# Kernel tuning notes

Measured on AMD Instinct MI355X. Metric: run time of the kernel, lower is better.

Reference implementation:

```python
import jax, jax.numpy as jnp
import numpy as np

B, S, IN, OUT, GS = 4, 2048, 4096, 4096, 256
NG = IN // GS  # number of groups per output channel


def setup_inputs() -> dict:
    key = jax.random.key(0)
    k1, k2, k3, k4 = jax.random.split(key, 4)
    x = jax.random.normal(k1, (B, S, IN), dtype=jnp.float32)
    # int4 codes stored in int8: values in [-8, 7]
    weight_int8 = jax.random.randint(k2, (OUT, IN), -8, 8, dtype=jnp.int32).astype(jnp.int8)
    scales = jax.random.uniform(k3, (OUT, NG), dtype=jnp.float32, minval=0.001, maxval=0.02)
    # zero points stored in scales_precision (float), integer-valued in int4 range
    zeros = jax.random.randint(k4, (OUT, NG), -8, 8, dtype=jnp.int32).astype(jnp.float32)
    return {"x": x, "weight_int8": weight_int8, "scales": scales, "zeros": zeros,
            "group_size": GS}


def per_token_dynamic_quant(x):
    """Asymmetric per-token int8 quantize -> dequantize (torchao decomposed ops)."""
    qmin, qmax = -128.0, 127.0
    mn = jnp.minimum(jnp.min(x, axis=-1, keepdims=True), 0.0)
    mx = jnp.maximum(jnp.max(x, axis=-1, keepdims=True), 0.0)
    eps = jnp.finfo(jnp.float32).eps
    scale = jnp.maximum((mx - mn) / (qmax - qmin), eps)
    # choose zero point minimizing error at whichever end is larger
    zp = jnp.where((qmin + mn / scale) + (qmax + mx / scale) > 0,
                   qmin - mn / scale, qmax - mx / scale)
    zp = jnp.clip(jnp.round(zp), qmin, qmax)
    q = jnp.clip(jnp.round(x / scale) + zp, qmin, qmax)
    return (q - zp) * scale


def dequant_per_channel_group(w_int8, scales, zeros, group_size):
    O, I = w_int8.shape
    g = I // group_size
    w = w_int8.reshape(O, g, group_size).astype(jnp.float32)
    w_dq = (w - zeros[:, :, None]) * scales[:, :, None]
    return w_dq.reshape(O, I)


def reference(x, weight_int8, scales, zeros, group_size):
    xq = per_token_dynamic_quant(x.astype(jnp.float32))
    w_dq = dequant_per_channel_group(weight_int8, scales, zeros, group_size)
    # F.linear: x @ w_dq.T  -> [B, S, OUT]
    return jnp.einsum('bsi,oi->bso', xq, w_dq)
```

## Files before the change

kernel.cpp:

```cpp
#include <hip/hip_runtime.h>
#include <hip/hip_bf16.h>
#include <stdint.h>

#define T_   8192
#define IN_  4096
#define OUT_ 4096
#define GS_  256
#define NG_  16

#define BM 128
#define BN 128
#define BK 128
#define KT (IN_ / BK)

typedef int   v4i __attribute__((ext_vector_type(4)));
typedef float f4  __attribute__((ext_vector_type(4)));

__device__ __forceinline__ void gload16(const void* g, void* l) {
  __builtin_amdgcn_global_load_lds(
      (const __attribute__((address_space(1))) void*)g,
      (__attribute__((address_space(3))) void*)l, 16, 0, 0);
}

__global__ __launch_bounds__(256) void quant_kernel(
    const float* __restrict__ x, int8_t* __restrict__ q,
    float* __restrict__ tscale, float* __restrict__ tzp) {
  const int t = blockIdx.x;
  const int tid = threadIdx.x;
  const float* xr = x + (size_t)t * IN_ + tid * 16;
  float vals[16];
  {
    f4 v0 = *(const f4*)(xr);
    f4 v1 = *(const f4*)(xr + 4);
    f4 v2 = *(const f4*)(xr + 8);
    f4 v3 = *(const f4*)(xr + 12);
#pragma unroll
    for (int i = 0; i < 4; ++i) {
      vals[i] = v0[i]; vals[4 + i] = v1[i]; vals[8 + i] = v2[i]; vals[12 + i] = v3[i];
    }
  }
  float mn = 0.f, mx = 0.f;
#pragma unroll
  for (int i = 0; i < 16; ++i) { mn = fminf(mn, vals[i]); mx = fmaxf(mx, vals[i]); }
#pragma unroll
  for (int off = 32; off > 0; off >>= 1) {
    mn = fminf(mn, __shfl_xor(mn, off));
    mx = fmaxf(mx, __shfl_xor(mx, off));
  }
  __shared__ float smn[4], smx[4];
  if ((tid & 63) == 0) { smn[tid >> 6] = mn; smx[tid >> 6] = mx; }
  __syncthreads();
  mn = fminf(fminf(smn[0], smn[1]), fminf(smn[2], smn[3]));
  mx = fmaxf(fmaxf(smx[0], smx[1]), fmaxf(smx[2], smx[3]));

  const float eps = 1.1920928955078125e-7f;
  float scale = fmaxf((mx - mn) / 255.0f, eps);
  float rmn = mn / scale;
  float rmx = mx / scale;
  float zp0 = ((-128.0f + rmn) + (127.0f + rmx) > 0.0f) ? (-128.0f - rmn)
                                                        : (127.0f - rmx);
  float zp = fminf(fmaxf(rintf(zp0), -128.0f), 127.0f);
  if (tid == 0) { tscale[t] = scale; tzp[t] = zp; }

  const float inv = 1.0f / scale;
  v4i packed;
#pragma unroll
  for (int w = 0; w < 4; ++w) {
    int word = 0;
#pragma unroll
    for (int e = 0; e < 4; ++e) {
      float qf = rintf(vals[w * 4 + e] * inv) + zp;
      qf = fminf(fmaxf(qf, -128.0f), 127.0f);
      int qi = (int)qf;
      word |= (qi & 0xff) << (8 * e);
    }
    packed[w] = word;
  }
  *(v4i*)(q + (size_t)t * IN_ + tid * 16) = packed;
}

__global__ __launch_bounds__(256) void wprep_kernel(
    const int* __restrict__ w, const float* __restrict__ scales,
    const float* __restrict__ zeros, int8_t* __restrict__ wq,
    float* __restrict__ c1) {
  const int o = blockIdx.x;
  const int tid = threadIdx.x;
  const int g = tid >> 4;
  const int* wr = w + (size_t)o * IN_ + tid * 16;
  const int zi = (int)zeros[o * NG_ + g];
  int ssum = 0;
  v4i packed;
#pragma unroll
  for (int blk = 0; blk < 4; ++blk) {
    v4i ww = *(const v4i*)(wr + blk * 4);
    int word = 0;
#pragma unroll
    for (int e = 0; e < 4; ++e) {
      int wp = ww[e] - zi;
      ssum += wp;
      word |= (wp & 0xff) << (8 * e);
    }
    packed[blk] = word;
  }
  *(v4i*)(wq + (size_t)o * IN_ + tid * 16) = packed;
  ssum += __shfl_xor(ssum, 1);
  ssum += __shfl_xor(ssum, 2);
  ssum += __shfl_xor(ssum, 4);
  ssum += __shfl_xor(ssum, 8);
  __shared__ float part[NG_];
  if ((tid & 15) == 0) part[g] = scales[o * NG_ + g] * (float)ssum;
  __syncthreads();
  if (tid == 0) {
    float s = 0.f;
#pragma unroll
    for (int i = 0; i < NG_; ++i) s += part[i];
    c1[o] = s;
  }
}

__global__ __launch_bounds__(256, 2) void gemm_kernel(
    const int8_t* __restrict__ q, const int8_t* __restrict__ wq,
    const float* __restrict__ scales, const float* __restrict__ tscale,
    const float* __restrict__ tzp, const float* __restrict__ c1,
    float* __restrict__ out) {
  __shared__ int8_t As[BM * BK];
  __shared__ int8_t Bs[BN * BK];
  __shared__ float sSc[NG_ * BN];

  const int tid = threadIdx.x;
  const int lane = tid & 63;
  const int wid = tid >> 6;
  const int R0 = blockIdx.y * BM;
  const int C0 = blockIdx.x * BN;

#pragma unroll
  for (int e = 0; e < 8; ++e) {
    int idx = tid + e * 256;
    int oc = idx >> 4, g = idx & 15;
    sSc[g * BN + oc] = scales[(size_t)(C0 + oc) * NG_ + g];
  }

  const int rA = tid >> 3;
  const int cswz = ((tid & 7) ^ (rA & 7)) * 16;
  const int8_t* gA = q + (size_t)(R0 + rA) * IN_ + cswz;
  const int8_t* gB = wq + (size_t)(C0 + rA) * IN_ + cswz;

  const int wm = (wid >> 1) * 64;
  const int wn = (wid & 1) * 64;
  const int lm = lane & 15;
  const int quad = lane >> 4;
  const int o0 = ((quad ^ (lm & 7)) * 16);
  const int aRow = (wm + lm) * BK;
  const int bRow = (wn + lm) * BK;

  v4i acci[4][4];
  float accf[4][4][4];
#pragma unroll
  for (int i = 0; i < 4; ++i)
#pragma unroll
    for (int j = 0; j < 4; ++j) {
      acci[i][j] = (v4i){0, 0, 0, 0};
#pragma unroll
      for (int r = 0; r < 4; ++r) accf[i][j][r] = 0.f;
    }

  for (int kt = 0; kt < KT; ++kt) {
    __syncthreads();
    const int koff = kt * BK;
#pragma unroll
    for (int i = 0; i < 4; ++i) {
      gload16(gA + koff + (size_t)(i * 32) * IN_, &As[i * 4096 + tid * 16]);
      gload16(gB + koff + (size_t)(i * 32) * IN_, &Bs[i * 4096 + tid * 16]);
    }
    __syncthreads();

#pragma unroll
    for (int ks = 0; ks < 2; ++ks) {
      const int co = o0 ^ (ks * 64);
      v4i af[4], bf[4];
#pragma unroll
      for (int i = 0; i < 4; ++i)
        af[i] = *(const v4i*)&As[aRow + i * (16 * BK) + co];
#pragma unroll
      for (int j = 0; j < 4; ++j)
        bf[j] = *(const v4i*)&Bs[bRow + j * (16 * BK) + co];
#pragma unroll
      for (int i = 0; i < 4; ++i)
#pragma unroll
        for (int j = 0; j < 4; ++j)
          acci[i][j] =
              __builtin_amdgcn_mfma_i32_16x16x64_i8(af[i], bf[j], acci[i][j], 0, 0, 0);
    }

    if (kt & 1) {
      const int g = kt >> 1;
      float sj[4];
#pragma unroll
      for (int j = 0; j < 4; ++j) sj[j] = sSc[g * BN + wn + j * 16 + lm];
#pragma unroll
      for (int i = 0; i < 4; ++i)
#pragma unroll
        for (int j = 0; j < 4; ++j) {
#pragma unroll
          for (int r = 0; r < 4; ++r)
            accf[i][j][r] += sj[j] * (float)acci[i][j][r];
          acci[i][j] = (v4i){0, 0, 0, 0};
        }
    }
  }

  float cj[4];
#pragma unroll
  for (int j = 0; j < 4; ++j) cj[j] = c1[C0 + wn + j * 16 + lm];
#pragma unroll
  for (int i = 0; i < 4; ++i) {
#pragma unroll
    for (int r = 0; r < 4; ++r) {
      const int row = R0 + wm + i * 16 + quad * 4 + r;
      const float tsc = tscale[row];
      const float tz = tzp[row];
#pragma unroll
      for (int j = 0; j < 4; ++j) {
        const int col = C0 + wn + j * 16 + lm;
        out[(size_t)row * OUT_ + col] = tsc * (accf[i][j][r] - tz * cj[j]);
      }
    }
  }
}

extern "C" void kernel_launch(void* const* d_in, const int* in_sizes, int n_in,
                              void* d_out, int out_size, void* d_ws, size_t ws_size,
                              hipStream_t stream) {
  const float* x = (const float*)d_in[0];
  const int* w = (const int*)d_in[1];
  const float* scales = (const float*)d_in[2];
  const float* zeros = (const float*)d_in[3];

  uint8_t* ws = (uint8_t*)d_ws;
  int8_t* q = (int8_t*)ws;
  int8_t* wq = (int8_t*)(ws + 33554432);
  float* tscale = (float*)(ws + 33554432 + 16777216);
  float* tzp = (float*)(ws + 33554432 + 16777216 + 32768);
  float* c1 = (float*)(ws + 33554432 + 16777216 + 65536);
  float* out = (float*)d_out;

  hipLaunchKernelGGL(quant_kernel, dim3(T_), dim3(256), 0, stream, x, q, tscale, tzp);
  hipLaunchKernelGGL(wprep_kernel, dim3(OUT_), dim3(256), 0, stream, w, scales, zeros, wq, c1);
  hipLaunchKernelGGL(gemm_kernel, dim3(OUT_ / BN, T_ / BM), dim3(256), 0, stream,
                     q, wq, scales, tscale, tzp, c1, out);
}
```

Baseline: 430.9 us.

## Double-buffer LDS tiles, widen to 256x128 with 8 waves, swizzle block order

The int8 GEMM tile grows to BN=256 with 512 threads (8 waves, 2x4 layout). LDS tiles are double-buffered, so global-to-LDS loads for the next K step are issued while MFMAs run on the current buffer. The block index is remapped across XCD groups for better L2 reuse, and setprio/s_barrier bracket the MFMA phases. The cost is more LDS (about 112KB per block), which may limit occupancy to one block per CU despite launch_bounds(512,2).

```diff
diff --git a/kernel.cpp b/kernel.cpp
--- a/kernel.cpp
+++ b/kernel.cpp
@@ -9,9 +9,12 @@
 #define NG_  16
 
 #define BM 128
-#define BN 128
+#define BN 256
 #define BK 128
 #define KT (IN_ / BK)
+#define GX (OUT_ / BN)
+#define GY (T_ / BM)
+#define NWG (GX * GY)
 
 typedef int   v4i __attribute__((ext_vector_type(4)));
 typedef float f4  __attribute__((ext_vector_type(4)));
@@ -118,38 +121,41 @@
   }
 }
 
-__global__ __launch_bounds__(256, 2) void gemm_kernel(
+__global__ __launch_bounds__(512, 2) void gemm_kernel(
     const int8_t* __restrict__ q, const int8_t* __restrict__ wq,
     const float* __restrict__ scales, const float* __restrict__ tscale,
     const float* __restrict__ tzp, const float* __restrict__ c1,
     float* __restrict__ out) {
-  __shared__ int8_t As[BM * BK];
-  __shared__ int8_t Bs[BN * BK];
+  __shared__ int8_t As[2][BM * BK];
+  __shared__ int8_t Bs[2][BN * BK];
   __shared__ float sSc[NG_ * BN];
 
   const int tid = threadIdx.x;
   const int lane = tid & 63;
   const int wid = tid >> 6;
-  const int R0 = blockIdx.y * BM;
-  const int C0 = blockIdx.x * BN;
+
+  const int orig = blockIdx.y * GX + blockIdx.x;
+  const int swz = (orig & 7) * (NWG / 8) + (orig >> 3);
+  const int R0 = (swz >> 4) * BM;
+  const int C0 = (swz & 15) * BN;
 
 #pragma unroll
   for (int e = 0; e < 8; ++e) {
-    int idx = tid + e * 256;
+    int idx = tid + e * 512;
     int oc = idx >> 4, g = idx & 15;
     sSc[g * BN + oc] = scales[(size_t)(C0 + oc) * NG_ + g];
   }
 
   const int rA = tid >> 3;
-  const int cswz = ((tid & 7) ^ (rA & 7)) * 16;
-  const int8_t* gA = q + (size_t)(R0 + rA) * IN_ + cswz;
-  const int8_t* gB = wq + (size_t)(C0 + rA) * IN_ + cswz;
-
-  const int wm = (wid >> 1) * 64;
-  const int wn = (wid & 1) * 64;
+  const int csw = ((tid & 7) ^ (rA & 7)) * 16;
+  const int8_t* gA = q + (size_t)(R0 + rA) * IN_ + csw;
+  const int8_t* gB = wq + (size_t)(C0 + rA) * IN_ + csw;
+
+  const int wm = (wid >> 2) * 64;
+  const int wn = (wid & 3) * 64;
   const int lm = lane & 15;
   const int quad = lane >> 4;
-  const int o0 = ((quad ^ (lm & 7)) * 16);
+  const int o0 = (quad ^ (lm & 7)) * 16;
   const int aRow = (wm + lm) * BK;
   const int bRow = (wn + lm) * BK;
 
@@ -164,33 +170,66 @@
       for (int r = 0; r < 4; ++r) accf[i][j][r] = 0.f;
     }
 
+#pragma unroll
+  for (int i = 0; i < 2; ++i)
+    gload16(gA + (size_t)(i * 64) * IN_, &As[0][i * 8192 + tid * 16]);
+#pragma unroll
+  for (int i = 0; i < 4; ++i)
+    gload16(gB + (size_t)(i * 64) * IN_, &Bs[0][i * 8192 + tid * 16]);
+  __syncthreads();
+
+  int cur = 0;
   for (int kt = 0; kt < KT; ++kt) {
-    __syncthreads();
-    const int koff = kt * BK;
-#pragma unroll
-    for (int i = 0; i < 4; ++i) {
-      gload16(gA + koff + (size_t)(i * 32) * IN_, &As[i * 4096 + tid * 16]);
-      gload16(gB + koff + (size_t)(i * 32) * IN_, &Bs[i * 4096 + tid * 16]);
-    }
-    __syncthreads();
-
-#pragma unroll
-    for (int ks = 0; ks < 2; ++ks) {
-      const int co = o0 ^ (ks * 64);
-      v4i af[4], bf[4];
-#pragma unroll
-      for (int i = 0; i < 4; ++i)
-        af[i] = *(const v4i*)&As[aRow + i * (16 * BK) + co];
-#pragma unroll
-      for (int j = 0; j < 4; ++j)
-        bf[j] = *(const v4i*)&Bs[bRow + j * (16 * BK) + co];
-#pragma unroll
-      for (int i = 0; i < 4; ++i)
-#pragma unroll
-        for (int j = 0; j < 4; ++j)
-          acci[i][j] =
-              __builtin_amdgcn_mfma_i32_16x16x64_i8(af[i], bf[j], acci[i][j], 0, 0, 0);
-    }
+    v4i af[4], bf[4];
+    {
+      const int co = o0;
+#pragma unroll
+      for (int i = 0; i < 4; ++i)
+        af[i] = *(const v4i*)&As[cur][aRow + i * (16 * BK) + co];
+#pragma unroll
+      for (int j = 0; j < 4; ++j)
+        bf[j] = *(const v4i*)&Bs[cur][bRow + j * (16 * BK) + co];
+    }
+    if (kt + 1 < KT) {
+      const size_t koff = (size_t)(kt + 1) * BK;
+#pragma unroll
+      for (int i = 0; i < 2; ++i)
+        gload16(gA + koff + (size_t)(i * 64) * IN_,
+                &As[cur ^ 1][i * 8192 + tid * 16]);
+#pragma unroll
+      for (int i = 0; i < 4; ++i)
+        gload16(gB + koff + (size_t)(i * 64) * IN_,
+                &Bs[cur ^ 1][i * 8192 + tid * 16]);
+    }
+    __builtin_amdgcn_s_barrier();
+    __builtin_amdgcn_s_setprio(1);
+#pragma unroll
+    for (int i = 0; i < 4; ++i)
+#pragma unroll
+      for (int j = 0; j < 4; ++j)
+        acci[i][j] =
+            __builtin_amdgcn_mfma_i32_16x16x64_i8(af[i], bf[j], acci[i][j], 0, 0, 0);
+    __builtin_amdgcn_s_setprio(0);
+    __builtin_amdgcn_s_barrier();
+
+    {
+      const int co = o0 ^ 64;
+#pragma unroll
+      for (int i = 0; i < 4; ++i)
+        af[i] = *(const v4i*)&As[cur][aRow + i * (16 * BK) + co];
+#pragma unroll
+      for (int j = 0; j < 4; ++j)
+        bf[j] = *(const v4i*)&Bs[cur][bRow + j * (16 * BK) + co];
+    }
+    __builtin_amdgcn_s_barrier();
+    __builtin_amdgcn_s_setprio(1);
+#pragma unroll
+    for (int i = 0; i < 4; ++i)
+#pragma unroll
+      for (int j = 0; j < 4; ++j)
+        acci[i][j] =
+            __builtin_amdgcn_mfma_i32_16x16x64_i8(af[i], bf[j], acci[i][j], 0, 0, 0);
+    __builtin_amdgcn_s_setprio(0);
 
     if (kt & 1) {
       const int g = kt >> 1;
@@ -207,6 +246,8 @@
           acci[i][j] = (v4i){0, 0, 0, 0};
         }
     }
+    __syncthreads();
+    cur ^= 1;
   }
 
   float cj[4];
@@ -246,6 +287,6 @@
 
   hipLaunchKernelGGL(quant_kernel, dim3(T_), dim3(256), 0, stream, x, q, tscale, tzp);
   hipLaunchKernelGGL(wprep_kernel, dim3(OUT_), dim3(256), 0, stream, w, scales, zeros, wq, c1);
-  hipLaunchKernelGGL(gemm_kernel, dim3(OUT_ / BN, T_ / BM), dim3(256), 0, stream,
+  hipLaunchKernelGGL(gemm_kernel, dim3(GX, GY), dim3(512), 0, stream,
                      q, wq, scales, tscale, tzp, c1, out);
 }
```

After: 473.5 us. +9.9%, slower.

## Double-buffer A tile in LDS and load B fragments directly into registers

Applied to the files above, without the earlier changes.

The GEMM now double-buffers the activation tile in LDS. It prefetches the next k-tile's activations with global_load_lds while computing the current one, so each iteration needs one barrier instead of two. Weight fragments are no longer staged through LDS; each lane loads its B operand straight from global memory into registers, one tile ahead. The grid is also transposed so consecutive blocks walk down rows and share a weight column tile. The cost is higher register pressure, since the launch-bounds occupancy hint is dropped, plus uncoalesced per-lane global loads for weights.

```diff
diff --git a/kernel.cpp b/kernel.cpp
--- a/kernel.cpp
+++ b/kernel.cpp
@@ -118,20 +118,19 @@
   }
 }
 
-__global__ __launch_bounds__(256, 2) void gemm_kernel(
+__global__ __launch_bounds__(256) void gemm_kernel(
     const int8_t* __restrict__ q, const int8_t* __restrict__ wq,
     const float* __restrict__ scales, const float* __restrict__ tscale,
     const float* __restrict__ tzp, const float* __restrict__ c1,
     float* __restrict__ out) {
-  __shared__ int8_t As[BM * BK];
-  __shared__ int8_t Bs[BN * BK];
+  __shared__ int8_t As[2][BM * BK];
   __shared__ float sSc[NG_ * BN];
 
   const int tid = threadIdx.x;
   const int lane = tid & 63;
   const int wid = tid >> 6;
-  const int R0 = blockIdx.y * BM;
-  const int C0 = blockIdx.x * BN;
+  const int R0 = blockIdx.x * BM;
+  const int C0 = blockIdx.y * BN;
 
 #pragma unroll
   for (int e = 0; e < 8; ++e) {
@@ -143,7 +142,6 @@
   const int rA = tid >> 3;
   const int cswz = ((tid & 7) ^ (rA & 7)) * 16;
   const int8_t* gA = q + (size_t)(R0 + rA) * IN_ + cswz;
-  const int8_t* gB = wq + (size_t)(C0 + rA) * IN_ + cswz;
 
   const int wm = (wid >> 1) * 64;
   const int wn = (wid & 1) * 64;
@@ -151,7 +149,8 @@
   const int quad = lane >> 4;
   const int o0 = ((quad ^ (lm & 7)) * 16);
   const int aRow = (wm + lm) * BK;
-  const int bRow = (wn + lm) * BK;
+
+  const int8_t* bBase = wq + (size_t)(C0 + wn + lm) * IN_ + quad * 16;
 
   v4i acci[4][4];
   float accf[4][4][4];
@@ -164,50 +163,80 @@
       for (int r = 0; r < 4; ++r) accf[i][j][r] = 0.f;
     }
 
-  for (int kt = 0; kt < KT; ++kt) {
-    __syncthreads();
-    const int koff = kt * BK;
-#pragma unroll
-    for (int i = 0; i < 4; ++i) {
-      gload16(gA + koff + (size_t)(i * 32) * IN_, &As[i * 4096 + tid * 16]);
-      gload16(gB + koff + (size_t)(i * 32) * IN_, &Bs[i * 4096 + tid * 16]);
-    }
-    __syncthreads();
-
-#pragma unroll
-    for (int ks = 0; ks < 2; ++ks) {
-      const int co = o0 ^ (ks * 64);
-      v4i af[4], bf[4];
-#pragma unroll
-      for (int i = 0; i < 4; ++i)
-        af[i] = *(const v4i*)&As[aRow + i * (16 * BK) + co];
-#pragma unroll
-      for (int j = 0; j < 4; ++j)
-        bf[j] = *(const v4i*)&Bs[bRow + j * (16 * BK) + co];
-#pragma unroll
-      for (int i = 0; i < 4; ++i)
-#pragma unroll
-        for (int j = 0; j < 4; ++j)
-          acci[i][j] =
-              __builtin_amdgcn_mfma_i32_16x16x64_i8(af[i], bf[j], acci[i][j], 0, 0, 0);
-    }
-
-    if (kt & 1) {
-      const int g = kt >> 1;
-      float sj[4];
-#pragma unroll
-      for (int j = 0; j < 4; ++j) sj[j] = sSc[g * BN + wn + j * 16 + lm];
-#pragma unroll
-      for (int i = 0; i < 4; ++i)
-#pragma unroll
-        for (int j = 0; j < 4; ++j) {
-#pragma unroll
-          for (int r = 0; r < 4; ++r)
-            accf[i][j][r] += sj[j] * (float)acci[i][j][r];
-          acci[i][j] = (v4i){0, 0, 0, 0};
-        }
-    }
-  }
+#define GEMM_BODY(KT_I, BC0, BC1, BNX0, BNX1, ACUR, ANEXT, DO_FOLD)           \
+  {                                                                           \
+    if ((KT_I) + 1 < KT) {                                                    \
+      const int8_t* bk = bBase + (size_t)((KT_I) + 1) * BK;                   \
+      _Pragma("unroll")                                                       \
+      for (int j = 0; j < 4; ++j) {                                           \
+        BNX0[j] = *(const v4i*)(bk + (size_t)j * (16 * IN_));                 \
+        BNX1[j] = *(const v4i*)(bk + (size_t)j * (16 * IN_) + 64);            \
+      }                                                                       \
+      const size_t koff = (size_t)((KT_I) + 1) * BK;                          \
+      _Pragma("unroll")                                                       \
+      for (int i = 0; i < 4; ++i)                                             \
+        gload16(gA + koff + (size_t)(i * 32) * IN_,                           \
+                &(ANEXT)[i * 4096 + tid * 16]);                               \
+    }                                                                         \
+    {                                                                         \
+      v4i af[4];                                                              \
+      _Pragma("unroll")                                                       \
+      for (int i = 0; i < 4; ++i)                                             \
+        af[i] = *(const v4i*)&(ACUR)[aRow + i * (16 * BK) + o0];              \
+      _Pragma("unroll")                                                       \
+      for (int i = 0; i < 4; ++i)                                             \
+        _Pragma("unroll")                                                     \
+        for (int j = 0; j < 4; ++j)                                           \
+          acci[i][j] = __builtin_amdgcn_mfma_i32_16x16x64_i8(                 \
+              af[i], BC0[j], acci[i][j], 0, 0, 0);                            \
+    }                                                                         \
+    {                                                                         \
+      const int co = o0 ^ 64;                                                 \
+      v4i af[4];                                                              \
+      _Pragma("unroll")                                                       \
+      for (int i = 0; i < 4; ++i)                                             \
+        af[i] = *(const v4i*)&(ACUR)[aRow + i * (16 * BK) + co];              \
+      _Pragma("unroll")                                                       \
+      for (int i = 0; i < 4; ++i)                                             \
+        _Pragma("unroll")                                                     \
+        for (int j = 0; j < 4; ++j)                                           \
+          acci[i][j] = __builtin_amdgcn_mfma_i32_16x16x64_i8(                 \
+              af[i], BC1[j], acci[i][j], 0, 0, 0);                            \
+    }                                                                         \
+    if (DO_FOLD) {                                                            \
+      const int g = (KT_I) >> 1;                                              \
+      float sj[4];                                                            \
+      _Pragma("unroll")                                                       \
+      for (int j = 0; j < 4; ++j) sj[j] = sSc[g * BN + wn + j * 16 + lm];     \
+      _Pragma("unroll")                                                       \
+      for (int i = 0; i < 4; ++i)                                             \
+        _Pragma("unroll")                                                     \
+        for (int j = 0; j < 4; ++j) {                                         \
+          _Pragma("unroll")                                                   \
+          for (int r = 0; r < 4; ++r)                                         \
+            accf[i][j][r] += sj[j] * (float)acci[i][j][r];                    \
+          acci[i][j] = (v4i){0, 0, 0, 0};                                     \
+        }                                                                     \
+    }                                                                         \
+    __syncthreads();                                                          \
+  }
+
+  v4i bfA0[4], bfA1[4], bfB0[4], bfB1[4];
+#pragma unroll
+  for (int j = 0; j < 4; ++j) {
+    bfA0[j] = *(const v4i*)(bBase + (size_t)j * (16 * IN_));
+    bfA1[j] = *(const v4i*)(bBase + (size_t)j * (16 * IN_) + 64);
+  }
+#pragma unroll
+  for (int i = 0; i < 4; ++i)
+    gload16(gA + (size_t)(i * 32) * IN_, &As[0][i * 4096 + tid * 16]);
+  __syncthreads();
+
+  for (int kt = 0; kt < KT; kt += 2) {
+    GEMM_BODY(kt,     bfA0, bfA1, bfB0, bfB1, As[0], As[1], false)
+    GEMM_BODY(kt + 1, bfB0, bfB1, bfA0, bfA1, As[1], As[0], true)
+  }
+#undef GEMM_BODY
 
   float cj[4];
 #pragma unroll
@@ -246,6 +275,6 @@
 
   hipLaunchKernelGGL(quant_kernel, dim3(T_), dim3(256), 0, stream, x, q, tscale, tzp);
   hipLaunchKernelGGL(wprep_kernel, dim3(OUT_), dim3(256), 0, stream, w, scales, zeros, wq, c1);
-  hipLaunchKernelGGL(gemm_kernel, dim3(OUT_ / BN, T_ / BM), dim3(256), 0, stream,
+  hipLaunchKernelGGL(gemm_kernel, dim3(T_ / BM, OUT_ / BN), dim3(256), 0, stream,
                      q, wq, scales, tscale, tzp, c1, out);
 }
```

Result: slower. 567.0 us (+31.6%).
